# Kernel tuning notes

Hardware: AMD Instinct MI355X
Metric: run time of the kernel (lower is better)

## Reference

```python
import jax, jax.numpy as jnp
import numpy as np

B, C, V = 4096, 1000, 8000   # batch, NUM_COMPO, NUM_CHARS
THRESH = 0.8                 # compo_score_thresh
SCALE = 0.1                  # score_adjustment_scale
TOPK = 5


def setup_inputs() -> dict:
    key = jax.random.key(0)
    k1, k2, k3, k4 = jax.random.split(key, 4)
    return {
        "pred_class_logits": jax.random.normal(k1, (B, V), jnp.float32),
        "pred_compo_logits": jax.random.normal(k2, (B, C), jnp.float32),
        "compo_co_occurrence_prob": jax.random.uniform(k3, (C, C), dtype=jnp.float32),
        "compo_chinese_matrix": jax.random.randint(k4, (C, V), 0, 2, dtype=jnp.int32),
    }


def _decode_one(compo_scores, co_occ, matrix):
    """components_to_chinese_char for one sample. compo_scores:[C], co_occ:[C,C], matrix:[C,V]."""
    nC, nV = matrix.shape
    # score adjustment from co-occurrence of components above threshold
    sel = compo_scores > THRESH                                   # [C]
    adj = SCALE * jnp.sum(
        jnp.where(sel[:, None], co_occ * compo_scores[:, None], 0.0), axis=0)  # [C]
    scores = compo_scores + adj
    max_idx = jnp.argmax(scores)
    max_score = scores[max_idx]
    # re-threshold and sort selected scores descending (fixed-shape: mask with -inf)
    sel2 = scores > THRESH
    num_selected = jnp.sum(sel2.astype(jnp.int32))
    masked = jnp.where(sel2, scores, -jnp.inf)
    order = jnp.argsort(-masked)          # descending; selected compo indices first
    sorted_scores = masked[order]
    hit0 = matrix[max_idx]                # [V] 0/1

    def cond(carry):
        i, hit, _ = carry
        return (i < num_selected) & (jnp.sum(hit) > 1)

    def body(carry):
        i, hit, _ = carry
        row = matrix[order[i]]
        new_hit = jnp.where(hit + row == 2, 1, 0).astype(jnp.int32)  # intersection
        return (i + 1, new_hit, hit)

    i0 = jnp.array(1, jnp.int32)
    i, hit, prev = jax.lax.while_loop(cond, body, (i0, hit0, hit0))
    empty = jnp.sum(hit) == 0
    i = jnp.where(empty, i - 1, i)
    hit = jnp.where(empty, prev, hit)
    hit_score = jnp.where(i == 1, max_score, sorted_scores[jnp.maximum(i - 1, 0)])
    # first 5 hit char indices (ascending, as tf.where yields), padded with -1
    char_ids = jnp.where(hit == 1, jnp.arange(nV), nV)
    first5 = jnp.sort(char_ids)[:TOPK]
    hit_indices = jnp.where(first5 == nV, -1, first5).astype(jnp.int32)
    return hit_indices, hit_score


def reference(pred_class_logits, pred_compo_logits, compo_co_occurrence_prob, compo_chinese_matrix):
    class_probs = jax.nn.softmax(pred_class_logits, axis=1)            # [B,V]
    class_scores, class_indices = jax.lax.top_k(class_probs, TOPK)     # [B,5]
    compo_scores = jax.nn.sigmoid(pred_compo_logits)                   # [B,C]
    hit_indices, hit_scores = jax.vmap(_decode_one, in_axes=(0, None, None))(
        compo_scores, compo_co_occurrence_prob, compo_chinese_matrix)
    class_indices = class_indices.astype(jnp.int32)
    num_hit = jnp.sum((hit_indices != -1).astype(jnp.int32), axis=1)   # [B]
    combined1 = jnp.where(num_hit == 1, hit_indices[:, 0], class_indices[:, 0])
    combined2 = jnp.where((class_scores[:, 0] < 0.85) & (num_hit == 1),
                          hit_indices[:, 0], class_indices[:, 0])
    return (class_indices, class_scores, hit_indices, hit_scores, combined1, combined2)
```

## Files before the change

kernel.cpp:

```cpp
#include <hip/hip_runtime.h>
#include <cstdint>
#include <cstddef>

typedef unsigned long long u64;

#define B_SZ 4096
#define C_SZ 1000
#define V_SZ 8000
#define RW 128
#define THRESHF 0.8f
#define SCALEF 0.1f

#define OFF_CI 0
#define OFF_CS (B_SZ * 5)
#define OFF_HI (2 * B_SZ * 5)
#define OFF_HS (3 * B_SZ * 5)
#define OFF_C1 (3 * B_SZ * 5 + B_SZ)
#define OFF_C2 (3 * B_SZ * 5 + 2 * B_SZ)

__global__ __launch_bounds__(256) void pack_kernel(const int* __restrict__ mat,
                                                   u64* __restrict__ packed) {
  const int c = blockIdx.x;
  const int tid = threadIdx.x;
  const int lane = tid & 63;
  const int wv = tid >> 6;
  const int* row = mat + (size_t)c * V_SZ;
  for (int base = 0; base < 8192; base += 256) {
    const int k = base + tid;
    int v = 0;
    if (k < V_SZ) v = row[k];
    u64 msk = __ballot(v != 0);
    if (lane == 0) packed[(size_t)c * RW + ((base >> 6) + wv)] = msk;
  }
}

__global__ __launch_bounds__(256) void class_topk_kernel(const float* __restrict__ logits,
                                                         float* __restrict__ out) {
  const int b = blockIdx.x;
  const int tid = threadIdx.x;
  const int lane = tid & 63;
  const int wv = tid >> 6;
  const float* row = logits + (size_t)b * V_SZ;
  float v[32];
#pragma unroll
  for (int f = 0; f < 8; ++f) {
    const int base = (f << 10) + (tid << 2);
    if (base < V_SZ) {
      float4 x = *(const float4*)(row + base);
      v[4 * f + 0] = x.x; v[4 * f + 1] = x.y; v[4 * f + 2] = x.z; v[4 * f + 3] = x.w;
    } else {
      v[4 * f + 0] = -INFINITY; v[4 * f + 1] = -INFINITY;
      v[4 * f + 2] = -INFINITY; v[4 * f + 3] = -INFINITY;
    }
  }
  __shared__ float sred[4];
  __shared__ int sredi[4];
  float lm = -INFINITY;
#pragma unroll
  for (int q = 0; q < 32; ++q) lm = fmaxf(lm, v[q]);
#pragma unroll
  for (int o = 32; o >= 1; o >>= 1) lm = fmaxf(lm, __shfl_xor(lm, o));
  if (lane == 0) sred[wv] = lm;
  __syncthreads();
  const float m = fmaxf(fmaxf(sred[0], sred[1]), fmaxf(sred[2], sred[3]));
  float ls = 0.f;
#pragma unroll
  for (int q = 0; q < 32; ++q) ls += expf(v[q] - m);
#pragma unroll
  for (int o = 32; o >= 1; o >>= 1) ls += __shfl_xor(ls, o);
  __syncthreads();
  if (lane == 0) sred[wv] = ls;
  __syncthreads();
  const float ssum = sred[0] + sred[1] + sred[2] + sred[3];
  for (int r = 0; r < 5; ++r) {
    float bv = -INFINITY;
    int bi = 0;
#pragma unroll
    for (int q = 0; q < 32; ++q) {
      const int idx = ((q >> 2) << 10) + (tid << 2) + (q & 3);
      if (v[q] > bv) { bv = v[q]; bi = idx; }
    }
#pragma unroll
    for (int o = 32; o >= 1; o >>= 1) {
      float ov = __shfl_xor(bv, o);
      int oi = __shfl_xor(bi, o);
      if (ov > bv || (ov == bv && oi < bi)) { bv = ov; bi = oi; }
    }
    __syncthreads();
    if (lane == 0) { sred[wv] = bv; sredi[wv] = bi; }
    __syncthreads();
    bv = sred[0]; bi = sredi[0];
#pragma unroll
    for (int w = 1; w < 4; ++w) {
      if (sred[w] > bv || (sred[w] == bv && sredi[w] < bi)) { bv = sred[w]; bi = sredi[w]; }
    }
    if (((bi & 1023) >> 2) == tid) {
      const int sl = ((bi >> 10) << 2) | (bi & 3);
#pragma unroll
      for (int q = 0; q < 32; ++q)
        if (q == sl) v[q] = -INFINITY;
    }
    if (tid == 0) {
      out[OFF_CI + b * 5 + r] = (float)bi;
      out[OFF_CS + b * 5 + r] = expf(bv - m) / ssum;
    }
  }
}

__global__ __launch_bounds__(256, 4) void decode_kernel(const float* __restrict__ compo_logits,
                                                        const float* __restrict__ co_occ,
                                                        const u64* __restrict__ packed,
                                                        float* __restrict__ out) {
  const int tid = threadIdx.x;
  const int lane = tid & 63;
  const int w = tid >> 6;
  const int b = blockIdx.x * 4 + w;
  __shared__ short s_idx[4][512];
  __shared__ float s_val[4][512];

  const float4* lg4 = (const float4*)(compo_logits + (size_t)b * C_SZ);
  float raw[16];
#pragma unroll
  for (int p = 0; p < 4; ++p) {
    const int fi = lane + (p << 6);
    if (fi < 250) {
      float4 x = lg4[fi];
      raw[4 * p + 0] = 1.0f / (1.0f + expf(-x.x));
      raw[4 * p + 1] = 1.0f / (1.0f + expf(-x.y));
      raw[4 * p + 2] = 1.0f / (1.0f + expf(-x.z));
      raw[4 * p + 3] = 1.0f / (1.0f + expf(-x.w));
    } else {
      raw[4 * p + 0] = 0.f; raw[4 * p + 1] = 0.f; raw[4 * p + 2] = 0.f; raw[4 * p + 3] = 0.f;
    }
  }
  int n = 0;
#pragma unroll
  for (int p = 0; p < 4; ++p) {
    unsigned mb = 0;
    if (raw[4 * p + 0] > THRESHF) mb |= 1u;
    if (raw[4 * p + 1] > THRESHF) mb |= 2u;
    if (raw[4 * p + 2] > THRESHF) mb |= 4u;
    if (raw[4 * p + 3] > THRESHF) mb |= 8u;
    const int cnt = __popc(mb);
    int inc = cnt;
#pragma unroll
    for (int o = 1; o < 64; o <<= 1) {
      int t = __shfl_up(inc, o);
      if (lane >= o) inc += t;
    }
    int off = n + inc - cnt;
    const int total = __shfl(inc, 63);
#pragma unroll
    for (int j = 0; j < 4; ++j) {
      if (mb & (1u << j)) {
        s_idx[w][off] = (short)((p << 8) + (lane << 2) + j);
        s_val[w][off] = raw[4 * p + j];
        ++off;
      }
    }
    n += total;
  }
  if (lane == 0) { s_idx[w][n] = 0; s_val[w][n] = 0.0f; }

  float4 acc0 = {0, 0, 0, 0}, acc1 = {0, 0, 0, 0}, acc2 = {0, 0, 0, 0}, acc3 = {0, 0, 0, 0};
  if (n > 0) {
    float mcur = s_val[w][0];
    float4 c0, c1, c2, c3 = {0, 0, 0, 0};
    {
      const float4* rp = (const float4*)(co_occ + (size_t)s_idx[w][0] * C_SZ);
      c0 = rp[lane]; c1 = rp[lane + 64]; c2 = rp[lane + 128];
      if (lane < 58) c3 = rp[lane + 192];
    }
    for (int e = 0; e < n; ++e) {
      const int inxt = s_idx[w][e + 1];
      const float mnxt = s_val[w][e + 1];
      float4 n0 = {0, 0, 0, 0}, n1 = {0, 0, 0, 0}, n2 = {0, 0, 0, 0}, n3 = {0, 0, 0, 0};
      const float4* rp = (const float4*)(co_occ + (size_t)inxt * C_SZ);
      n0 = rp[lane]; n1 = rp[lane + 64]; n2 = rp[lane + 128];
      if (lane < 58) n3 = rp[lane + 192];
      acc0.x += mcur * c0.x; acc0.y += mcur * c0.y; acc0.z += mcur * c0.z; acc0.w += mcur * c0.w;
      acc1.x += mcur * c1.x; acc1.y += mcur * c1.y; acc1.z += mcur * c1.z; acc1.w += mcur * c1.w;
      acc2.x += mcur * c2.x; acc2.y += mcur * c2.y; acc2.z += mcur * c2.z; acc2.w += mcur * c2.w;
      acc3.x += mcur * c3.x; acc3.y += mcur * c3.y; acc3.z += mcur * c3.z; acc3.w += mcur * c3.w;
      c0 = n0; c1 = n1; c2 = n2; c3 = n3;
      mcur = mnxt;
    }
  }
  float fin[16];
  fin[0] = raw[0] + SCALEF * acc0.x;  fin[1] = raw[1] + SCALEF * acc0.y;
  fin[2] = raw[2] + SCALEF * acc0.z;  fin[3] = raw[3] + SCALEF * acc0.w;
  fin[4] = raw[4] + SCALEF * acc1.x;  fin[5] = raw[5] + SCALEF * acc1.y;
  fin[6] = raw[6] + SCALEF * acc1.z;  fin[7] = raw[7] + SCALEF * acc1.w;
  fin[8] = raw[8] + SCALEF * acc2.x;  fin[9] = raw[9] + SCALEF * acc2.y;
  fin[10] = raw[10] + SCALEF * acc2.z; fin[11] = raw[11] + SCALEF * acc2.w;
  fin[12] = raw[12] + SCALEF * acc3.x; fin[13] = raw[13] + SCALEF * acc3.y;
  fin[14] = raw[14] + SCALEF * acc3.z; fin[15] = raw[15] + SCALEF * acc3.w;

  u64 key[16];
  unsigned avail = 0;
  int cnt = 0;
  u64 kb = 0;
#pragma unroll
  for (int q = 0; q < 16; ++q) {
    const int col = (lane << 2) + (q & 3) + ((q >> 2) << 8);
    if (col < C_SZ) {
      const float f = fin[q];
      const u64 k = ((u64)__float_as_uint(f) << 32) | (u64)(0xFFFFFFFFu - (unsigned)col);
      key[q] = k;
      if (k > kb) kb = k;
      if (f > THRESHF) { avail |= 1u << q; cnt++; }
    } else key[q] = 0;
  }
  u64 mk = kb;
#pragma unroll
  for (int o = 32; o >= 1; o >>= 1) { u64 t = __shfl_xor(mk, o); if (t > mk) mk = t; }
  const float mxv = __uint_as_float((unsigned)(mk >> 32));
  const int mxi = (int)(0xFFFFFFFFu - (unsigned)(mk & 0xFFFFFFFFull));
#pragma unroll
  for (int o = 32; o >= 1; o >>= 1) cnt += __shfl_xor(cnt, o);
  const int nsel = cnt;
  if (((mxi >> 2) & 63) == lane) avail &= ~(1u << ((mxi & 3) | ((mxi >> 8) << 2)));
  const u64* pr = packed + (size_t)mxi * RW;
  u64 h0 = pr[lane], h1 = pr[64 + lane];
  int pc = __popcll(h0) + __popcll(h1);
#pragma unroll
  for (int o = 32; o >= 1; o >>= 1) pc += __shfl_xor(pc, o);
  int ii = 1;
  float last_val = mxv;
  if (nsel >= 2 && pc > 1) {
    for (;;) {
      int kt = (nsel - ii < 8) ? (nsel - ii) : 8;
      float cval[8];
      int cidx[8];
      u64 rl[8], rh[8];
      float lastc = last_val;
      int kv = 0;
#pragma unroll
      for (int k = 0; k < 8; ++k) {
        cval[k] = 0.0f; cidx[k] = -1;
        if (k < kt) {
          u64 lm = 0;
#pragma unroll
          for (int q = 0; q < 16; ++q)
            if (avail & (1u << q)) { if (key[q] > lm) lm = key[q]; }
          u64 ck = lm;
#pragma unroll
          for (int o = 32; o >= 1; o >>= 1) { u64 t = __shfl_xor(ck, o); if (t > ck) ck = t; }
          if (ck != 0) {
            cval[k] = __uint_as_float((unsigned)(ck >> 32));
            cidx[k] = (int)(0xFFFFFFFFu - (unsigned)(ck & 0xFFFFFFFFull));
            if (((cidx[k] >> 2) & 63) == lane)
              avail &= ~(1u << ((cidx[k] & 3) | ((cidx[k] >> 8) << 2)));
            lastc = cval[k];
            kv = k + 1;
          }
        }
      }
      kt = kv;
      if (kt == 0) break;
#pragma unroll
      for (int k = 0; k < 8; ++k) {
        if (k < kt) {
          const u64* rp2 = packed + (size_t)cidx[k] * RW;
          rl[k] = rp2[lane]; rh[k] = rp2[64 + lane];
        } else { rl[k] = ~0ull; rh[k] = ~0ull; }
      }
      u64 c0 = h0, c1 = h1, pk0 = 0, pk1 = 0;
#pragma unroll
      for (int k = 0; k < 8; ++k) {
        c0 &= rl[k]; c1 &= rh[k];
        const u64 p = (u64)(__popcll(c0) + __popcll(c1));
        if (k < 4) pk0 |= p << (k * 16); else pk1 |= p << ((k - 4) * 16);
      }
#pragma unroll
      for (int o = 32; o >= 1; o >>= 1) { pk0 += __shfl_xor(pk0, o); pk1 += __shfl_xor(pk1, o); }
      int kstar = -1;
      unsigned pcv = 0;
#pragma unroll
      for (int k = 0; k < 8; ++k) {
        if (k < kt && kstar < 0) {
          const unsigned f = (unsigned)(((k < 4 ? pk0 : pk1) >> ((k & 3) * 16)) & 0xFFFFull);
          if (f <= 1u) { kstar = k; pcv = f; }
        }
      }
      if (kstar >= 0) {
        float vk = 0.f, vkm1 = last_val;
#pragma unroll
        for (int k = 0; k < 8; ++k)
          if (k == kstar) { vk = cval[k]; if (k > 0) vkm1 = cval[k - 1]; }
        const int na = (pcv == 1u) ? (kstar + 1) : kstar;
#pragma unroll
        for (int k = 0; k < 8; ++k) if (k < na) { h0 &= rl[k]; h1 &= rh[k]; }
        if (pcv == 1u) { ii += kstar + 1; last_val = vk; }
        else { ii += kstar; last_val = vkm1; }
        break;
      }
#pragma unroll
      for (int k = 0; k < 8; ++k) if (k < kt) { h0 &= rl[k]; h1 &= rh[k]; }
      ii += kt;
      last_val = lastc;
      if (ii >= nsel) break;
    }
  }
  const float hit_score = (ii == 1) ? mxv : last_val;

  const int c0n = __popcll(h0), c1n = __popcll(h1);
  int s0 = c0n;
#pragma unroll
  for (int o = 1; o < 64; o <<= 1) {
    int nn = __shfl_up(s0, o);
    if (lane >= o) s0 += nn;
  }
  const int tot0 = __shfl(s0, 63);
  const int pre0 = s0 - c0n;
  int s1 = c1n;
#pragma unroll
  for (int o = 1; o < 64; o <<= 1) {
    int nn = __shfl_up(s1, o);
    if (lane >= o) s1 += nn;
  }
  const int tot = tot0 + __shfl(s1, 63);
  const int pre1 = tot0 + s1 - c1n;
  {
    u64 x = h0;
    int r = pre0;
    while (x && r < 5) {
      const int bp = __ffsll((unsigned long long)x) - 1;
      out[OFF_HI + b * 5 + r] = (float)((lane << 6) + bp);
      x &= x - 1;
      ++r;
    }
    x = h1;
    r = pre1;
    while (x && r < 5) {
      const int bp = __ffsll((unsigned long long)x) - 1;
      out[OFF_HI + b * 5 + r] = (float)(((64 + lane) << 6) + bp);
      x &= x - 1;
      ++r;
    }
  }
  int fb = 0x7fffffff;
  if (c0n) fb = (lane << 6) + __ffsll((unsigned long long)h0) - 1;
  else if (c1n) fb = ((64 + lane) << 6) + __ffsll((unsigned long long)h1) - 1;
#pragma unroll
  for (int o = 32; o >= 1; o >>= 1) fb = min(fb, __shfl_xor(fb, o));
  if (lane == 0) {
    const int num_hit = tot < 5 ? tot : 5;
    for (int r = num_hit; r < 5; ++r) out[OFF_HI + b * 5 + r] = -1.0f;
    out[OFF_HS + b] = hit_score;
    const float ci0 = out[OFF_CI + b * 5];
    const float cs0 = out[OFF_CS + b * 5];
    out[OFF_C1 + b] = (num_hit == 1) ? (float)fb : ci0;
    out[OFF_C2 + b] = (cs0 < 0.85f && num_hit == 1) ? (float)fb : ci0;
  }
}

extern "C" void kernel_launch(void* const* d_in, const int* in_sizes, int n_in,
                              void* d_out, int out_size, void* d_ws, size_t ws_size,
                              hipStream_t stream) {
  (void)in_sizes; (void)n_in; (void)out_size; (void)ws_size;
  const float* class_logits = (const float*)d_in[0];
  const float* compo_logits = (const float*)d_in[1];
  const float* co_occ = (const float*)d_in[2];
  const int* mat = (const int*)d_in[3];
  float* out = (float*)d_out;
  u64* packed = (u64*)d_ws;

  pack_kernel<<<C_SZ, 256, 0, stream>>>(mat, packed);
  class_topk_kernel<<<B_SZ, 256, 0, stream>>>(class_logits, out);
  decode_kernel<<<B_SZ / 4, 256, 0, stream>>>(compo_logits, co_occ, packed, out);
}
```

Measured before the change: 134.7 us.

## Split decode into column-halved matvec kernel and separate tail kernel

The fused decode kernel is split in two. A matvec kernel computes the adjusted scores, with each sample's columns divided across two blocks (halves), unrolled by two rows, and run at higher occupancy, then writes them to a workspace buffer. A separate tail kernel reads the scores back in a lane-strided layout and performs the serial intersection search. This trades extra global traffic and a kernel launch for more parallelism and occupancy in the bandwidth-bound co-occurrence gather.

```diff
diff --git a/kernel.cpp b/kernel.cpp
--- a/kernel.cpp
+++ b/kernel.cpp
@@ -107,14 +107,18 @@
   }
 }
 
-__global__ __launch_bounds__(256, 4) void decode_kernel(const float* __restrict__ compo_logits,
+__global__ __launch_bounds__(256, 8) void matvec_kernel(const float* __restrict__ compo_logits,
                                                         const float* __restrict__ co_occ,
-                                                        const u64* __restrict__ packed,
-                                                        float* __restrict__ out) {
+                                                        float* __restrict__ fin_ws) {
   const int tid = threadIdx.x;
   const int lane = tid & 63;
   const int w = tid >> 6;
-  const int b = blockIdx.x * 4 + w;
+  const int bid = blockIdx.x;
+  const int g = bid >> 3;
+  const int r = bid & 7;
+  const int h = r >> 2;
+  const int sg = g * 4 + (r & 3);
+  const int b = sg * 4 + w;
   __shared__ short s_idx[4][512];
   __shared__ float s_val[4][512];
 
@@ -160,55 +164,67 @@
     }
     n += total;
   }
-  if (lane == 0) { s_idx[w][n] = 0; s_val[w][n] = 0.0f; }
-
-  float4 acc0 = {0, 0, 0, 0}, acc1 = {0, 0, 0, 0}, acc2 = {0, 0, 0, 0}, acc3 = {0, 0, 0, 0};
-  if (n > 0) {
-    float mcur = s_val[w][0];
-    float4 c0, c1, c2, c3 = {0, 0, 0, 0};
-    {
-      const float4* rp = (const float4*)(co_occ + (size_t)s_idx[w][0] * C_SZ);
-      c0 = rp[lane]; c1 = rp[lane + 64]; c2 = rp[lane + 128];
-      if (lane < 58) c3 = rp[lane + 192];
-    }
-    for (int e = 0; e < n; ++e) {
-      const int inxt = s_idx[w][e + 1];
-      const float mnxt = s_val[w][e + 1];
-      float4 n0 = {0, 0, 0, 0}, n1 = {0, 0, 0, 0}, n2 = {0, 0, 0, 0}, n3 = {0, 0, 0, 0};
-      const float4* rp = (const float4*)(co_occ + (size_t)inxt * C_SZ);
-      n0 = rp[lane]; n1 = rp[lane + 64]; n2 = rp[lane + 128];
-      if (lane < 58) n3 = rp[lane + 192];
-      acc0.x += mcur * c0.x; acc0.y += mcur * c0.y; acc0.z += mcur * c0.z; acc0.w += mcur * c0.w;
-      acc1.x += mcur * c1.x; acc1.y += mcur * c1.y; acc1.z += mcur * c1.z; acc1.w += mcur * c1.w;
-      acc2.x += mcur * c2.x; acc2.y += mcur * c2.y; acc2.z += mcur * c2.z; acc2.w += mcur * c2.w;
-      acc3.x += mcur * c3.x; acc3.y += mcur * c3.y; acc3.z += mcur * c3.z; acc3.w += mcur * c3.w;
-      c0 = n0; c1 = n1; c2 = n2; c3 = n3;
-      mcur = mnxt;
-    }
-  }
-  float fin[16];
-  fin[0] = raw[0] + SCALEF * acc0.x;  fin[1] = raw[1] + SCALEF * acc0.y;
-  fin[2] = raw[2] + SCALEF * acc0.z;  fin[3] = raw[3] + SCALEF * acc0.w;
-  fin[4] = raw[4] + SCALEF * acc1.x;  fin[5] = raw[5] + SCALEF * acc1.y;
-  fin[6] = raw[6] + SCALEF * acc1.z;  fin[7] = raw[7] + SCALEF * acc1.w;
-  fin[8] = raw[8] + SCALEF * acc2.x;  fin[9] = raw[9] + SCALEF * acc2.y;
-  fin[10] = raw[10] + SCALEF * acc2.z; fin[11] = raw[11] + SCALEF * acc2.w;
-  fin[12] = raw[12] + SCALEF * acc3.x; fin[13] = raw[13] + SCALEF * acc3.y;
-  fin[14] = raw[14] + SCALEF * acc3.z; fin[15] = raw[15] + SCALEF * acc3.w;
-
+  if (lane < 2) { s_idx[w][n + lane] = 0; s_val[w][n + lane] = 0.0f; }
+
+  float4 accA = {0, 0, 0, 0}, accB = {0, 0, 0, 0};
+  {
+    const float4* cop = (const float4*)co_occ;
+    const int f4a = (h << 7) + lane;
+    const int f4b = f4a + 64;
+    const bool gb = (h == 0) || (lane < 58);
+    for (int e = 0; e < n; e += 2) {
+      const int i0 = s_idx[w][e + 0]; const float m0 = s_val[w][e + 0];
+      const int i1 = s_idx[w][e + 1]; const float m1 = s_val[w][e + 1];
+      const float4* r0 = cop + (size_t)i0 * 250;
+      const float4* r1 = cop + (size_t)i1 * 250;
+      const float4 a0 = r0[f4a];
+      const float4 a1 = r1[f4a];
+      float4 b0 = {0, 0, 0, 0}, b1 = {0, 0, 0, 0};
+      if (gb) { b0 = r0[f4b]; b1 = r1[f4b]; }
+      accA.x += m0 * a0.x; accA.y += m0 * a0.y; accA.z += m0 * a0.z; accA.w += m0 * a0.w;
+      accB.x += m0 * b0.x; accB.y += m0 * b0.y; accB.z += m0 * b0.z; accB.w += m0 * b0.w;
+      accA.x += m1 * a1.x; accA.y += m1 * a1.y; accA.z += m1 * a1.z; accA.w += m1 * a1.w;
+      accB.x += m1 * b1.x; accB.y += m1 * b1.y; accB.z += m1 * b1.z; accB.w += m1 * b1.w;
+    }
+  }
+  float* dst = fin_ws + (size_t)b * C_SZ;
+  float4 oA, oB;
+  if (h == 0) {
+    oA.x = raw[0] + SCALEF * accA.x; oA.y = raw[1] + SCALEF * accA.y;
+    oA.z = raw[2] + SCALEF * accA.z; oA.w = raw[3] + SCALEF * accA.w;
+    oB.x = raw[4] + SCALEF * accB.x; oB.y = raw[5] + SCALEF * accB.y;
+    oB.z = raw[6] + SCALEF * accB.z; oB.w = raw[7] + SCALEF * accB.w;
+    *(float4*)(dst + (lane << 2)) = oA;
+    *(float4*)(dst + 256 + (lane << 2)) = oB;
+  } else {
+    oA.x = raw[8] + SCALEF * accA.x;  oA.y = raw[9] + SCALEF * accA.y;
+    oA.z = raw[10] + SCALEF * accA.z; oA.w = raw[11] + SCALEF * accA.w;
+    oB.x = raw[12] + SCALEF * accB.x; oB.y = raw[13] + SCALEF * accB.y;
+    oB.z = raw[14] + SCALEF * accB.z; oB.w = raw[15] + SCALEF * accB.w;
+    *(float4*)(dst + 512 + (lane << 2)) = oA;
+    if (lane < 58) *(float4*)(dst + 768 + (lane << 2)) = oB;
+  }
+}
+
+__global__ __launch_bounds__(256, 4) void tail_kernel(const float* __restrict__ sc_arr,
+                                                      const u64* __restrict__ packed,
+                                                      float* __restrict__ out) {
+  const int b = blockIdx.x * 4 + (threadIdx.x >> 6);
+  const int lane = threadIdx.x & 63;
+  const float* sc = sc_arr + (size_t)b * C_SZ;
   u64 key[16];
   unsigned avail = 0;
   int cnt = 0;
   u64 kb = 0;
 #pragma unroll
   for (int q = 0; q < 16; ++q) {
-    const int col = (lane << 2) + (q & 3) + ((q >> 2) << 8);
+    const int col = lane + (q << 6);
     if (col < C_SZ) {
-      const float f = fin[q];
-      const u64 k = ((u64)__float_as_uint(f) << 32) | (u64)(0xFFFFFFFFu - (unsigned)col);
+      const float s = sc[col];
+      const u64 k = ((u64)__float_as_uint(s) << 32) | (u64)(0xFFFFFFFFu - (unsigned)col);
       key[q] = k;
       if (k > kb) kb = k;
-      if (f > THRESHF) { avail |= 1u << q; cnt++; }
+      if (s > THRESHF) { avail |= 1u << q; cnt++; }
     } else key[q] = 0;
   }
   u64 mk = kb;
@@ -219,17 +235,17 @@
 #pragma unroll
   for (int o = 32; o >= 1; o >>= 1) cnt += __shfl_xor(cnt, o);
   const int nsel = cnt;
-  if (((mxi >> 2) & 63) == lane) avail &= ~(1u << ((mxi & 3) | ((mxi >> 8) << 2)));
+  if ((mxi & 63) == lane) avail &= ~(1u << (mxi >> 6));
   const u64* pr = packed + (size_t)mxi * RW;
   u64 h0 = pr[lane], h1 = pr[64 + lane];
   int pc = __popcll(h0) + __popcll(h1);
 #pragma unroll
   for (int o = 32; o >= 1; o >>= 1) pc += __shfl_xor(pc, o);
-  int ii = 1;
+  int i = 1;
   float last_val = mxv;
   if (nsel >= 2 && pc > 1) {
     for (;;) {
-      int kt = (nsel - ii < 8) ? (nsel - ii) : 8;
+      int kt = (nsel - i < 8) ? (nsel - i) : 8;
       float cval[8];
       int cidx[8];
       u64 rl[8], rh[8];
@@ -249,8 +265,7 @@
           if (ck != 0) {
             cval[k] = __uint_as_float((unsigned)(ck >> 32));
             cidx[k] = (int)(0xFFFFFFFFu - (unsigned)(ck & 0xFFFFFFFFull));
-            if (((cidx[k] >> 2) & 63) == lane)
-              avail &= ~(1u << ((cidx[k] & 3) | ((cidx[k] >> 8) << 2)));
+            if ((cidx[k] & 63) == lane) avail &= ~(1u << (cidx[k] >> 6));
             lastc = cval[k];
             kv = k + 1;
           }
@@ -261,8 +276,8 @@
 #pragma unroll
       for (int k = 0; k < 8; ++k) {
         if (k < kt) {
-          const u64* rp2 = packed + (size_t)cidx[k] * RW;
-          rl[k] = rp2[lane]; rh[k] = rp2[64 + lane];
+          const u64* rp = packed + (size_t)cidx[k] * RW;
+          rl[k] = rp[lane]; rh[k] = rp[64 + lane];
         } else { rl[k] = ~0ull; rh[k] = ~0ull; }
       }
       u64 c0 = h0, c1 = h1, pk0 = 0, pk1 = 0;
@@ -291,33 +306,33 @@
         const int na = (pcv == 1u) ? (kstar + 1) : kstar;
 #pragma unroll
         for (int k = 0; k < 8; ++k) if (k < na) { h0 &= rl[k]; h1 &= rh[k]; }
-        if (pcv == 1u) { ii += kstar + 1; last_val = vk; }
-        else { ii += kstar; last_val = vkm1; }
+        if (pcv == 1u) { i += kstar + 1; last_val = vk; }
+        else { i += kstar; last_val = vkm1; }
         break;
       }
 #pragma unroll
       for (int k = 0; k < 8; ++k) if (k < kt) { h0 &= rl[k]; h1 &= rh[k]; }
-      ii += kt;
+      i += kt;
       last_val = lastc;
-      if (ii >= nsel) break;
-    }
-  }
-  const float hit_score = (ii == 1) ? mxv : last_val;
+      if (i >= nsel) break;
+    }
+  }
+  const float hit_score = (i == 1) ? mxv : last_val;
 
   const int c0n = __popcll(h0), c1n = __popcll(h1);
   int s0 = c0n;
 #pragma unroll
   for (int o = 1; o < 64; o <<= 1) {
-    int nn = __shfl_up(s0, o);
-    if (lane >= o) s0 += nn;
+    int n = __shfl_up(s0, o);
+    if (lane >= o) s0 += n;
   }
   const int tot0 = __shfl(s0, 63);
   const int pre0 = s0 - c0n;
   int s1 = c1n;
 #pragma unroll
   for (int o = 1; o < 64; o <<= 1) {
-    int nn = __shfl_up(s1, o);
-    if (lane >= o) s1 += nn;
+    int n = __shfl_up(s1, o);
+    if (lane >= o) s1 += n;
   }
   const int tot = tot0 + __shfl(s1, 63);
   const int pre1 = tot0 + s1 - c1n;
@@ -365,8 +380,10 @@
   const int* mat = (const int*)d_in[3];
   float* out = (float*)d_out;
   u64* packed = (u64*)d_ws;
+  float* fin_ws = (float*)((char*)d_ws + (size_t)C_SZ * RW * 8);
 
   pack_kernel<<<C_SZ, 256, 0, stream>>>(mat, packed);
   class_topk_kernel<<<B_SZ, 256, 0, stream>>>(class_logits, out);
-  decode_kernel<<<B_SZ / 4, 256, 0, stream>>>(compo_logits, co_occ, packed, out);
-}
+  matvec_kernel<<<B_SZ / 2, 256, 0, stream>>>(compo_logits, co_occ, fin_ws);
+  tail_kernel<<<B_SZ / 4, 256, 0, stream>>>(fin_ws, packed, out);
+}
```

New measurement: 148.6 us. 10.3% more time.
